# Kernel optimization log

Hardware: AMD Instinct MI355X
Metric: run time of the kernel (lower is better)

## Reference

```python
import jax, jax.numpy as jnp
import numpy as np

B, T, E = 4096, 200, 64
H = E
A = [4 * E, 80, 40]  # attn_hidden_units


def setup_inputs() -> dict:
    key = jax.random.key(0)
    ks = jax.random.split(key, 16)
    s = 0.05
    inp = {
        "gru_outputs": jax.random.normal(ks[0], (B, T, E), jnp.float32),
        "targets": jax.random.normal(ks[1], (B, 1, E), jnp.float32),
        # attention MLP: 256 -> 80 -> 40 -> 1
        "W1": jax.random.normal(ks[2], (A[0], A[1]), jnp.float32) * s,
        "b1": jnp.zeros((A[1],), jnp.float32),
        "W2": jax.random.normal(ks[3], (A[1], A[2]), jnp.float32) * s,
        "b2": jnp.zeros((A[2],), jnp.float32),
        "Wf": jax.random.normal(ks[4], (A[2], 1), jnp.float32) * s,
        "bf": jnp.zeros((1,), jnp.float32),
        # GRU cell: update/reset gates map (E+H) -> 1, candidate -> H
        "Wu": jax.random.normal(ks[5], (E + H, 1), jnp.float32) * s,
        "bu": jnp.zeros((1,), jnp.float32),
        "Wr": jax.random.normal(ks[6], (E + H, 1), jnp.float32) * s,
        "br": jnp.zeros((1,), jnp.float32),
        "Wc": jax.random.normal(ks[7], (E + H, H), jnp.float32) * s,
        "bc": jnp.zeros((H,), jnp.float32),
    }
    return inp


def reference(gru_outputs, targets, W1, b1, W2, b2, Wf, bf, Wu, bu, Wr, br, Wc, bc):
    # --- LocalActivationUnit: scores over history ---
    k = gru_outputs                                   # [B,T,E]
    q = jnp.broadcast_to(targets, k.shape)            # repeat target along T
    x = jnp.concatenate([q, k, q - k, q * k], -1)     # [B,T,4E]
    x = x @ W1 + b1                                   # (no activation in source)
    x = x @ W2 + b2
    logits = x @ Wf + bf                              # [B,T,1]
    logits = jnp.where(logits == 0, -jnp.inf, logits)  # masked_fill(logits==0, -inf)
    scores = jax.nn.softmax(logits, axis=0)           # softmax over batch dim (dim=0, as in source)

    # --- AUGRU recurrence over time ---
    def step(h, xt):
        xi, si = xt                                   # [B,E], [B,1]
        cat = jnp.concatenate([xi, h], -1)            # [B,E+H]
        u = si * jax.nn.sigmoid(cat @ Wu + bu)        # [B,1]
        r = jax.nn.sigmoid(cat @ Wr + br)             # [B,1]
        cat2 = jnp.concatenate([xi, h * r], -1)
        tilde_h = jnp.tanh(cat2 @ Wc + bc)            # [B,H]
        h = (1 - u) * h + u * tilde_h
        return h, None

    h0 = jnp.zeros((gru_outputs.shape[0], H), gru_outputs.dtype)
    xs = (jnp.swapaxes(gru_outputs, 0, 1), jnp.swapaxes(scores, 0, 1))  # [T,B,*]
    hT, _ = jax.lax.scan(step, h0, xs)
    return hT
```

## Files before the change

kernel.cpp:

```cpp
#include <hip/hip_runtime.h>
#include <hip/hip_bf16.h>
#include <math.h>

#define BB 4096
#define TT 200
#define EE 64

#define OFF_XG 1976320
#define OFF_XC 3614720
#define WS_NEED_BYTES ((size_t)(OFF_XC + (size_t)BB * TT * 64) * 4)

__device__ __forceinline__ float lane_bcast(float v, int l) {
    return __int_as_float(__builtin_amdgcn_readlane(__float_as_int(v), l));
}

__device__ __forceinline__ float dpp_ror_add(float s, const int ctrl) {
    int t;
    switch (ctrl) {
        case 8: t = __builtin_amdgcn_update_dpp(0, __float_as_int(s), 0x128, 0xF, 0xF, true); break;
        case 4: t = __builtin_amdgcn_update_dpp(0, __float_as_int(s), 0x124, 0xF, 0xF, true); break;
        case 2: t = __builtin_amdgcn_update_dpp(0, __float_as_int(s), 0x122, 0xF, 0xF, true); break;
        default: t = __builtin_amdgcn_update_dpp(0, __float_as_int(s), 0x121, 0xF, 0xF, true); break;
    }
    return s + __int_as_float(t);
}

__device__ __forceinline__ float wave_sum64(float v) {
    v = dpp_ror_add(v, 8);
    v = dpp_ror_add(v, 4);
    v = dpp_ror_add(v, 2);
    v = dpp_ror_add(v, 1);
    v += __shfl_xor(v, 16);
    v += __shfl_xor(v, 32);
    return v;
}

__global__ __launch_bounds__(128) void weff_kernel(
    const float* __restrict__ W1, const float* __restrict__ b1,
    const float* __restrict__ W2, const float* __restrict__ b2,
    const float* __restrict__ Wf, const float* __restrict__ bf,
    float* __restrict__ ws) {
    __shared__ float t80[80];
    int tid = threadIdx.x;
    if (tid < 80) {
        float s = 0.0f;
        for (int j = 0; j < 40; j++) s = fmaf(W2[tid * 40 + j], Wf[j], s);
        t80[tid] = s;
    }
    __syncthreads();
    if (tid < 64) {
        float eq = 0.f, ek = 0.f, ed = 0.f, ep = 0.f;
        for (int m = 0; m < 80; m++) {
            float t = t80[m];
            eq = fmaf(W1[tid * 80 + m],         t, eq);
            ek = fmaf(W1[(64 + tid) * 80 + m],  t, ek);
            ed = fmaf(W1[(128 + tid) * 80 + m], t, ed);
            ep = fmaf(W1[(192 + tid) * 80 + m], t, ep);
        }
        ws[tid]       = ek - ed;
        ws[64 + tid]  = ep;
        ws[128 + tid] = eq + ed;
    } else if (tid == 64) {
        float s = bf[0];
        for (int m = 0; m < 80; m++) s = fmaf(b1[m], t80[m], s);
        for (int j = 0; j < 40; j++) s = fmaf(b2[j], Wf[j], s);
        ws[192] = s;
    }
}

__global__ __launch_bounds__(256) void logits_kernel(
    const float* __restrict__ gru, const float* __restrict__ targets,
    const float* __restrict__ ws, float* __restrict__ logits) {
    __shared__ float4 sA[16], sP[16], sQ[16];
    __shared__ float sc0;
    int tid = threadIdx.x;
    if (tid < 16) {
        sA[tid] = ((const float4*)ws)[tid];
        sP[tid] = ((const float4*)(ws + 64))[tid];
        sQ[tid] = ((const float4*)(ws + 128))[tid];
    }
    if (tid == 16) sc0 = ws[192];
    __syncthreads();

    int idx = blockIdx.x * 256 + tid;
    int b = idx / 200;
    int t = idx - b * 200;
    const float4* kp = (const float4*)(gru + ((size_t)b * 200 + t) * 64);
    const float4* qp = (const float4*)(targets + (size_t)b * 64);

    float a0 = sc0, a1 = 0.f, a2 = 0.f, a3 = 0.f;
#pragma unroll
    for (int i = 0; i < 16; i++) {
        float4 kv = kp[i], qv = qp[i], A = sA[i], P = sP[i], Q = sQ[i];
        a0 = fmaf(qv.x, Q.x, a0); a0 = fmaf(kv.x, fmaf(qv.x, P.x, A.x), a0);
        a1 = fmaf(qv.y, Q.y, a1); a1 = fmaf(kv.y, fmaf(qv.y, P.y, A.y), a1);
        a2 = fmaf(qv.z, Q.z, a2); a2 = fmaf(kv.z, fmaf(qv.z, P.z, A.z), a2);
        a3 = fmaf(qv.w, Q.w, a3); a3 = fmaf(kv.w, fmaf(qv.w, P.w, A.w), a3);
    }
    float lg = (a0 + a1) + (a2 + a3);
    if (lg == 0.0f) lg = -INFINITY;
    logits[(size_t)t * BB + b] = lg;
}

__global__ __launch_bounds__(256) void softmax_kernel(const float* __restrict__ logits,
                                                      float* __restrict__ scores) {
    int t = blockIdx.x;
    int tid = threadIdx.x;
    const float* L = logits + (size_t)t * BB;
    float v[16];
#pragma unroll
    for (int i = 0; i < 16; i++) {
        float x = L[tid + i * 256];
        v[i] = (x == 0.0f) ? -INFINITY : x;
    }
    float m = v[0];
#pragma unroll
    for (int i = 1; i < 16; i++) m = fmaxf(m, v[i]);
#pragma unroll
    for (int off = 32; off; off >>= 1) m = fmaxf(m, __shfl_xor(m, off));
    __shared__ float sm[4];
    __shared__ float ss[4];
    int wid = tid >> 6;
    if ((tid & 63) == 0) sm[wid] = m;
    __syncthreads();
    m = fmaxf(fmaxf(sm[0], sm[1]), fmaxf(sm[2], sm[3]));
    float e[16];
    float s = 0.0f;
#pragma unroll
    for (int i = 0; i < 16; i++) {
        e[i] = __expf(v[i] - m);
        s += e[i];
    }
#pragma unroll
    for (int off = 32; off; off >>= 1) s += __shfl_xor(s, off);
    if ((tid & 63) == 0) ss[wid] = s;
    __syncthreads();
    s = ss[0] + ss[1] + ss[2] + ss[3];
    float inv = 1.0f / s;
    float* S = scores + (size_t)t * BB;
#pragma unroll
    for (int i = 0; i < 16; i++) S[tid + i * 256] = e[i] * inv;
}

__global__ __launch_bounds__(256) void xprep_kernel(
    const float* __restrict__ gru, const float* __restrict__ Wc,
    const float* __restrict__ bc, const float* __restrict__ Wu,
    const float* __restrict__ Wr, float* __restrict__ xc,
    float* __restrict__ xg) {
    __shared__ float  Xs[32][65];
    __shared__ float4 Ws[1024];
    __shared__ float  Wg[128];
    const int tid = threadIdx.x;
    const int n0 = blockIdx.x * 32;
    const int nl = tid >> 3;
    const int qs = tid & 7;

    const float4* Wq = (const float4*)Wc;
#pragma unroll
    for (int i = 0; i < 4; i++) Ws[tid * 4 + i] = Wq[tid * 4 + i];
    if (tid < 128) Wg[tid] = (tid < 64) ? Wu[tid] : Wr[tid - 64];
    {
        const float4* gq = (const float4*)(gru + (size_t)(n0 + nl) * 64);
        float4 aa = gq[qs * 2];
        float4 bb = gq[qs * 2 + 1];
        float* xrow = &Xs[nl][qs * 8];
        xrow[0] = aa.x; xrow[1] = aa.y; xrow[2] = aa.z; xrow[3] = aa.w;
        xrow[4] = bb.x; xrow[5] = bb.y; xrow[6] = bb.z; xrow[7] = bb.w;
    }
    __syncthreads();

    const float4* bcq = (const float4*)bc;
    float4 acc0 = bcq[qs];
    float4 acc1 = bcq[qs + 8];
#pragma unroll
    for (int k = 0; k < 64; k++) {
        float  xk = Xs[nl][k];
        float4 w0 = Ws[k * 16 + qs];
        float4 w1 = Ws[k * 16 + qs + 8];
        acc0.x = fmaf(xk, w0.x, acc0.x);
        acc0.y = fmaf(xk, w0.y, acc0.y);
        acc0.z = fmaf(xk, w0.z, acc0.z);
        acc0.w = fmaf(xk, w0.w, acc0.w);
        acc1.x = fmaf(xk, w1.x, acc1.x);
        acc1.y = fmaf(xk, w1.y, acc1.y);
        acc1.z = fmaf(xk, w1.z, acc1.z);
        acc1.w = fmaf(xk, w1.w, acc1.w);
    }
    int n = n0 + nl;
    int b = n / 200;
    int t = n - b * 200;
    float4* o = (float4*)(xc + ((size_t)t * BB + b) * 64);
    o[qs]     = acc0;
    o[qs + 8] = acc1;
    if (qs == 0) {
        float su = 0.f, sr = 0.f;
#pragma unroll
        for (int k = 0; k < 64; k++) {
            float xk = Xs[nl][k];
            su = fmaf(xk, Wg[k], su);
            sr = fmaf(xk, Wg[64 + k], sr);
        }
        ((float2*)xg)[(size_t)t * BB + b] = make_float2(su, sr);
    }
}

__global__ __launch_bounds__(256, 2) void augru2_kernel(
    const float* __restrict__ xc, const float* __restrict__ xg,
    const float* __restrict__ scores,
    const float* __restrict__ Wu, const float* __restrict__ bu,
    const float* __restrict__ Wr, const float* __restrict__ br,
    const float* __restrict__ Wc, float* __restrict__ out) {
    __shared__ float hbuf[4][64];
    const int lane = threadIdx.x & 63;
    const int wid  = threadIdx.x >> 6;
    const int b    = blockIdx.x * 4 + wid;

    float wc2[64];
#pragma unroll
    for (int k = 0; k < 64; k++) wc2[k] = Wc[(64 + k) * 64 + lane];
    const float wu2l = Wu[64 + lane];
    const float wr2l = Wr[64 + lane];
    const float sbu = bu[0], sbr = br[0];
    const float2* xg2 = (const float2*)xg;

    float h = 0.0f;
    float  x0 = xc[(size_t)b * 64 + lane];
    float2 g0 = xg2[b];
    float  s0 = scores[b];
    size_t i1 = (size_t)BB + b;
    float  x1 = xc[i1 * 64 + lane];
    float2 g1 = xg2[i1];
    float  s1 = scores[i1];

    for (int t = 0; t < TT; t++) {
        float x2 = 0.0f, s2 = 0.0f;
        float2 g2 = make_float2(0.0f, 0.0f);
        if (t + 2 < TT) {
            size_t i2 = (size_t)(t + 2) * BB + b;
            x2 = xc[i2 * 64 + lane];
            g2 = xg2[i2];
            s2 = scores[i2];
        }

        hbuf[wid][lane] = h;

        float pu = wave_sum64(h * wu2l);
        float pr = wave_sum64(h * wr2l);
        float u = s0 / (1.0f + __expf(-(pu + g0.x + sbu)));
        float r = 1.0f / (1.0f + __expf(-(pr + g0.y + sbr)));

        float a0 = 0.f, a1 = 0.f, a2 = 0.f, a3 = 0.f;
        float a4 = 0.f, a5 = 0.f, a6 = 0.f, a7 = 0.f;
        const float4* h4 = (const float4*)hbuf[wid];
#pragma unroll
        for (int kq = 0; kq < 8; kq++) {
            float4 hv0 = h4[2 * kq];
            float4 hv1 = h4[2 * kq + 1];
            a0 = fmaf(hv0.x, wc2[8 * kq + 0], a0);
            a1 = fmaf(hv0.y, wc2[8 * kq + 1], a1);
            a2 = fmaf(hv0.z, wc2[8 * kq + 2], a2);
            a3 = fmaf(hv0.w, wc2[8 * kq + 3], a3);
            a4 = fmaf(hv1.x, wc2[8 * kq + 4], a4);
            a5 = fmaf(hv1.y, wc2[8 * kq + 5], a5);
            a6 = fmaf(hv1.z, wc2[8 * kq + 6], a6);
            a7 = fmaf(hv1.w, wc2[8 * kq + 7], a7);
        }
        float cand = ((a0 + a1) + (a2 + a3)) + ((a4 + a5) + (a6 + a7));
        float arg = x0 + r * cand;
        float ex = __expf(2.0f * arg);
        float th = 1.0f - 2.0f / (ex + 1.0f);
        h = fmaf(u, th - h, h);

        x0 = x1; g0 = g1; s0 = s1;
        x1 = x2; g1 = g2; s1 = s2;
    }
    out[(size_t)b * 64 + lane] = h;
}

__global__ __launch_bounds__(128, 4) void augru_kernel(
    const float* __restrict__ gru, const float* __restrict__ scores,
    const float* __restrict__ Wu, const float* __restrict__ bu,
    const float* __restrict__ Wr, const float* __restrict__ br,
    const float* __restrict__ Wc, const float* __restrict__ bc,
    float* __restrict__ out) {
    __shared__ float sxc[2][64];
    __shared__ float sxg[2][2];
    const int lane = threadIdx.x & 63;
    const int wid  = threadIdx.x >> 6;
    const int b    = blockIdx.x;
    const float* xrow = gru + (size_t)b * TT * 64;

    if (wid == 0) {
        float wc1[64];
#pragma unroll
        for (int k = 0; k < 64; k++) wc1[k] = Wc[k * 64 + lane];
        float wu1l = Wu[lane], wr1l = Wr[lane];
        float bcl = bc[lane];

        auto produce = [&](int tp, float xl) {
            float pu = xl * wu1l;
            float pr = xl * wr1l;
#pragma unroll
            for (int off = 32; off; off >>= 1) {
                pu += __shfl_xor(pu, off);
                pr += __shfl_xor(pr, off);
            }
            float a0 = bcl, a1 = 0.0f, a2 = 0.0f, a3 = 0.0f;
#pragma unroll
            for (int k = 0; k < 16; k++) {
                a0 = fmaf(lane_bcast(xl, 4 * k + 0), wc1[4 * k + 0], a0);
                a1 = fmaf(lane_bcast(xl, 4 * k + 1), wc1[4 * k + 1], a1);
                a2 = fmaf(lane_bcast(xl, 4 * k + 2), wc1[4 * k + 2], a2);
                a3 = fmaf(lane_bcast(xl, 4 * k + 3), wc1[4 * k + 3], a3);
            }
            int p = tp & 1;
            sxc[p][lane] = (a0 + a1) + (a2 + a3);
            if (lane == 0) sxg[p][0] = pu;
            if (lane == 1) sxg[p][1] = pr;
        };

        float xl = xrow[lane];
        float xn = xrow[64 + lane];
        produce(0, xl);
        xl = xn;
        __syncthreads();
        for (int t = 0; t < TT; t++) {
            if (t + 1 < TT) {
                float xnn = (t + 2 < TT) ? xrow[(size_t)(t + 2) * 64 + lane] : 0.0f;
                produce(t + 1, xl);
                xl = xnn;
            }
            __syncthreads();
        }
    } else {
        float wc2[64];
#pragma unroll
        for (int k = 0; k < 64; k++) wc2[k] = Wc[(64 + k) * 64 + lane];
        float wu2l = Wu[64 + lane], wr2l = Wr[64 + lane];
        float sbu = bu[0], sbr = br[0];
        float h = 0.0f;
        __syncthreads();
        for (int t = 0; t < TT; t++) {
            int p = t & 1;
            float sc = scores[(size_t)t * BB + b];
            float xcv = sxc[p][lane];
            float xu = sxg[p][0];
            float xv = sxg[p][1];
            float pu = h * wu2l;
            float pr = h * wr2l;
#pragma unroll
            for (int off = 32; off; off >>= 1) {
                pu += __shfl_xor(pu, off);
                pr += __shfl_xor(pr, off);
            }
            float u = sc / (1.0f + __expf(-(pu + xu + sbu)));
            float r = 1.0f / (1.0f + __expf(-(pr + xv + sbr)));
            float a0 = 0.0f, a1 = 0.0f, a2 = 0.0f, a3 = 0.0f;
#pragma unroll
            for (int k = 0; k < 16; k++) {
                a0 = fmaf(lane_bcast(h, 4 * k + 0), wc2[4 * k + 0], a0);
                a1 = fmaf(lane_bcast(h, 4 * k + 1), wc2[4 * k + 1], a1);
                a2 = fmaf(lane_bcast(h, 4 * k + 2), wc2[4 * k + 2], a2);
                a3 = fmaf(lane_bcast(h, 4 * k + 3), wc2[4 * k + 3], a3);
            }
            float arg = xcv + r * ((a0 + a1) + (a2 + a3));
            float ex = __expf(2.0f * arg);
            float th = 1.0f - 2.0f / (ex + 1.0f);
            h = fmaf(u, th - h, h);
            __syncthreads();
        }
        out[(size_t)b * 64 + lane] = h;
    }
}

extern "C" void kernel_launch(void* const* d_in, const int* in_sizes, int n_in,
                              void* d_out, int out_size, void* d_ws, size_t ws_size,
                              hipStream_t stream) {
    const float* gru     = (const float*)d_in[0];
    const float* targets = (const float*)d_in[1];
    const float* W1 = (const float*)d_in[2];
    const float* b1 = (const float*)d_in[3];
    const float* W2 = (const float*)d_in[4];
    const float* b2 = (const float*)d_in[5];
    const float* Wf = (const float*)d_in[6];
    const float* bf = (const float*)d_in[7];
    const float* Wu = (const float*)d_in[8];
    const float* bu = (const float*)d_in[9];
    const float* Wr = (const float*)d_in[10];
    const float* br = (const float*)d_in[11];
    const float* Wc = (const float*)d_in[12];
    const float* bc = (const float*)d_in[13];
    float* out = (float*)d_out;

    float* ws     = (float*)d_ws;
    float* logits = ws + 337920;
    float* scores = ws + 1157120;

    const bool big = (ws_size >= WS_NEED_BYTES);
    float* xg = ws + OFF_XG;
    float* xc = ws + OFF_XC;

    weff_kernel<<<1, 128, 0, stream>>>(W1, b1, W2, b2, Wf, bf, ws);
    logits_kernel<<<3200, 256, 0, stream>>>(gru, targets, ws, logits);
    softmax_kernel<<<200, 256, 0, stream>>>(logits, scores);
    if (big) {
        xprep_kernel<<<25600, 256, 0, stream>>>(gru, Wc, bc, Wu, Wr, xc, xg);
        augru2_kernel<<<1024, 256, 0, stream>>>(xc, xg, scores, Wu, bu, Wr, br, Wc, out);
    } else {
        augru_kernel<<<4096, 128, 0, stream>>>(gru, scores, Wu, bu, Wr, br, Wc, bc, out);
    }
}
```

Before: 844.3 us.

## Retile input projection, store xc batch-major, stage per-row gates/scores in LDS

The input projection kernel now processes 128 rows per block, with each thread computing a 4x8 register tile using packed two-wide FMAs. It writes xc in [B][T][64] order, so the recurrence kernel streams contiguous rows per batch element instead of striding across time. The recurrence kernel preloads scores and gate projections for all 200 steps into LDS. It packs the Wc recurrent weights into v2f registers and uses packed FMAs, dropping to launch_bounds(256,1). Fewer waves per SIMD reduces latency hiding in the serial recurrence, which is the main risk.

```diff
diff --git a/kernel.cpp b/kernel.cpp
--- a/kernel.cpp
+++ b/kernel.cpp
@@ -5,6 +5,8 @@
 #define BB 4096
 #define TT 200
 #define EE 64
+
+typedef float v2f __attribute__((ext_vector_type(2)));
 
 #define OFF_XG 1976320
 #define OFF_XC 3614720
@@ -142,138 +144,178 @@
     for (int i = 0; i < 16; i++) S[tid + i * 256] = e[i] * inv;
 }
 
+#define XPAD 68
 __global__ __launch_bounds__(256) void xprep_kernel(
     const float* __restrict__ gru, const float* __restrict__ Wc,
     const float* __restrict__ bc, const float* __restrict__ Wu,
     const float* __restrict__ Wr, float* __restrict__ xc,
     float* __restrict__ xg) {
-    __shared__ float  Xs[32][65];
-    __shared__ float4 Ws[1024];
-    __shared__ float  Wg[128];
+    __shared__ float Xs[128][XPAD];
+    __shared__ float Ws[64 * 64];
     const int tid = threadIdx.x;
-    const int n0 = blockIdx.x * 32;
-    const int nl = tid >> 3;
+    const int n0 = blockIdx.x * 128;
+
+    {
+        const float4* Wq = (const float4*)Wc;
+        float4* Wsq = (float4*)Ws;
+#pragma unroll
+        for (int i = 0; i < 4; i++) Wsq[tid + 256 * i] = Wq[tid + 256 * i];
+    }
+    {
+        int row = tid >> 1, half = tid & 1;
+        const float4* gq = (const float4*)(gru + (size_t)(n0 + row) * 64 + half * 32);
+#pragma unroll
+        for (int i = 0; i < 8; i++) {
+            *(float4*)&Xs[row][half * 32 + i * 4] = gq[i];
+        }
+    }
+    __syncthreads();
+
     const int qs = tid & 7;
-
-    const float4* Wq = (const float4*)Wc;
-#pragma unroll
-    for (int i = 0; i < 4; i++) Ws[tid * 4 + i] = Wq[tid * 4 + i];
-    if (tid < 128) Wg[tid] = (tid < 64) ? Wu[tid] : Wr[tid - 64];
+    const int g  = tid >> 3;
+
+    v2f acc[4][4];
     {
-        const float4* gq = (const float4*)(gru + (size_t)(n0 + nl) * 64);
-        float4 aa = gq[qs * 2];
-        float4 bb = gq[qs * 2 + 1];
-        float* xrow = &Xs[nl][qs * 8];
-        xrow[0] = aa.x; xrow[1] = aa.y; xrow[2] = aa.z; xrow[3] = aa.w;
-        xrow[4] = bb.x; xrow[5] = bb.y; xrow[6] = bb.z; xrow[7] = bb.w;
-    }
-    __syncthreads();
-
-    const float4* bcq = (const float4*)bc;
-    float4 acc0 = bcq[qs];
-    float4 acc1 = bcq[qs + 8];
-#pragma unroll
-    for (int k = 0; k < 64; k++) {
-        float  xk = Xs[nl][k];
-        float4 w0 = Ws[k * 16 + qs];
-        float4 w1 = Ws[k * 16 + qs + 8];
-        acc0.x = fmaf(xk, w0.x, acc0.x);
-        acc0.y = fmaf(xk, w0.y, acc0.y);
-        acc0.z = fmaf(xk, w0.z, acc0.z);
-        acc0.w = fmaf(xk, w0.w, acc0.w);
-        acc1.x = fmaf(xk, w1.x, acc1.x);
-        acc1.y = fmaf(xk, w1.y, acc1.y);
-        acc1.z = fmaf(xk, w1.z, acc1.z);
-        acc1.w = fmaf(xk, w1.w, acc1.w);
-    }
-    int n = n0 + nl;
-    int b = n / 200;
-    int t = n - b * 200;
-    float4* o = (float4*)(xc + ((size_t)t * BB + b) * 64);
-    o[qs]     = acc0;
-    o[qs + 8] = acc1;
-    if (qs == 0) {
-        float su = 0.f, sr = 0.f;
-#pragma unroll
-        for (int k = 0; k < 64; k++) {
-            float xk = Xs[nl][k];
-            su = fmaf(xk, Wg[k], su);
-            sr = fmaf(xk, Wg[64 + k], sr);
-        }
-        ((float2*)xg)[(size_t)t * BB + b] = make_float2(su, sr);
-    }
-}
-
-__global__ __launch_bounds__(256, 2) void augru2_kernel(
+        const v2f* bc2 = (const v2f*)(bc + qs * 8);
+        v2f b0 = bc2[0], b1 = bc2[1], b2v = bc2[2], b3 = bc2[3];
+#pragma unroll
+        for (int ri = 0; ri < 4; ri++) {
+            acc[ri][0] = b0; acc[ri][1] = b1; acc[ri][2] = b2v; acc[ri][3] = b3;
+        }
+    }
+
+#pragma unroll 4
+    for (int kc = 0; kc < 16; kc++) {
+        float4 xr[4];
+#pragma unroll
+        for (int ri = 0; ri < 4; ri++)
+            xr[ri] = *(const float4*)&Xs[g + 32 * ri][kc * 4];
+#pragma unroll
+        for (int kk = 0; kk < 4; kk++) {
+            const float4* wq = (const float4*)&Ws[(kc * 4 + kk) * 64 + qs * 8];
+            float4 wa = wq[0], wb = wq[1];
+            v2f w0 = {wa.x, wa.y}, w1 = {wa.z, wa.w};
+            v2f w2 = {wb.x, wb.y}, w3 = {wb.z, wb.w};
+#pragma unroll
+            for (int ri = 0; ri < 4; ri++) {
+                float xv = (kk == 0) ? xr[ri].x : (kk == 1) ? xr[ri].y
+                         : (kk == 2) ? xr[ri].z : xr[ri].w;
+                v2f xb = {xv, xv};
+                acc[ri][0] = __builtin_elementwise_fma(xb, w0, acc[ri][0]);
+                acc[ri][1] = __builtin_elementwise_fma(xb, w1, acc[ri][1]);
+                acc[ri][2] = __builtin_elementwise_fma(xb, w2, acc[ri][2]);
+                acc[ri][3] = __builtin_elementwise_fma(xb, w3, acc[ri][3]);
+            }
+        }
+    }
+
+#pragma unroll
+    for (int ri = 0; ri < 4; ri++) {
+        int n = n0 + g + 32 * ri;
+        float4 o0 = {acc[ri][0].x, acc[ri][0].y, acc[ri][1].x, acc[ri][1].y};
+        float4 o1 = {acc[ri][2].x, acc[ri][2].y, acc[ri][3].x, acc[ri][3].y};
+        float4* o = (float4*)(xc + (size_t)n * 64 + qs * 8);
+        o[0] = o0;
+        o[1] = o1;
+    }
+
+    {
+        int m = qs & 3;
+        int row = g + 32 * m;
+        const float* wsel = (qs >> 2) ? Wr : Wu;
+        const float4* wq = (const float4*)wsel;
+        float d0 = 0.f, d1 = 0.f, d2 = 0.f, d3 = 0.f;
+#pragma unroll
+        for (int i = 0; i < 16; i++) {
+            float4 xv = *(const float4*)&Xs[row][i * 4];
+            float4 wv = wq[i];
+            d0 = fmaf(xv.x, wv.x, d0);
+            d1 = fmaf(xv.y, wv.y, d1);
+            d2 = fmaf(xv.z, wv.z, d2);
+            d3 = fmaf(xv.w, wv.w, d3);
+        }
+        float dot = (d0 + d1) + (d2 + d3);
+        int n = n0 + row;
+        xg[(size_t)n * 2 + (qs >> 2)] = dot;
+    }
+}
+
+__global__ __launch_bounds__(256, 1) void augru3_kernel(
     const float* __restrict__ xc, const float* __restrict__ xg,
     const float* __restrict__ scores,
     const float* __restrict__ Wu, const float* __restrict__ bu,
     const float* __restrict__ Wr, const float* __restrict__ br,
     const float* __restrict__ Wc, float* __restrict__ out) {
-    __shared__ float hbuf[4][64];
+    __shared__ float  hbuf[4][64];
+    __shared__ float  ssc[4][200];
+    __shared__ float2 sxgl[4][200];
     const int lane = threadIdx.x & 63;
     const int wid  = threadIdx.x >> 6;
     const int b    = blockIdx.x * 4 + wid;
 
-    float wc2[64];
-#pragma unroll
-    for (int k = 0; k < 64; k++) wc2[k] = Wc[(64 + k) * 64 + lane];
+    const float2* xg2 = (const float2*)xg;
+    for (int t0 = lane; t0 < TT; t0 += 64) {
+        ssc[wid][t0]  = scores[(size_t)t0 * BB + b];
+        sxgl[wid][t0] = xg2[(size_t)b * TT + t0];
+    }
+
+    v2f wc[32];
+#pragma unroll
+    for (int m = 0; m < 32; m++) {
+        wc[m].x = Wc[(64 + 2 * m) * 64 + lane];
+        wc[m].y = Wc[(64 + 2 * m + 1) * 64 + lane];
+    }
     const float wu2l = Wu[64 + lane];
     const float wr2l = Wr[64 + lane];
     const float sbu = bu[0], sbr = br[0];
-    const float2* xg2 = (const float2*)xg;
 
     float h = 0.0f;
-    float  x0 = xc[(size_t)b * 64 + lane];
-    float2 g0 = xg2[b];
-    float  s0 = scores[b];
-    size_t i1 = (size_t)BB + b;
-    float  x1 = xc[i1 * 64 + lane];
-    float2 g1 = xg2[i1];
-    float  s1 = scores[i1];
-
-    for (int t = 0; t < TT; t++) {
-        float x2 = 0.0f, s2 = 0.0f;
-        float2 g2 = make_float2(0.0f, 0.0f);
-        if (t + 2 < TT) {
-            size_t i2 = (size_t)(t + 2) * BB + b;
-            x2 = xc[i2 * 64 + lane];
-            g2 = xg2[i2];
-            s2 = scores[i2];
-        }
-
-        hbuf[wid][lane] = h;
-
+    float* hb = hbuf[wid];
+    const float4* h4 = (const float4*)hb;
+    const float* ssw = ssc[wid];
+    const float2* sxw = sxgl[wid];
+
+    auto step = [&](int t, float xl) {
+        hb[lane] = h;
         float pu = wave_sum64(h * wu2l);
         float pr = wave_sum64(h * wr2l);
-        float u = s0 / (1.0f + __expf(-(pu + g0.x + sbu)));
-        float r = 1.0f / (1.0f + __expf(-(pr + g0.y + sbr)));
-
-        float a0 = 0.f, a1 = 0.f, a2 = 0.f, a3 = 0.f;
-        float a4 = 0.f, a5 = 0.f, a6 = 0.f, a7 = 0.f;
-        const float4* h4 = (const float4*)hbuf[wid];
-#pragma unroll
-        for (int kq = 0; kq < 8; kq++) {
-            float4 hv0 = h4[2 * kq];
-            float4 hv1 = h4[2 * kq + 1];
-            a0 = fmaf(hv0.x, wc2[8 * kq + 0], a0);
-            a1 = fmaf(hv0.y, wc2[8 * kq + 1], a1);
-            a2 = fmaf(hv0.z, wc2[8 * kq + 2], a2);
-            a3 = fmaf(hv0.w, wc2[8 * kq + 3], a3);
-            a4 = fmaf(hv1.x, wc2[8 * kq + 4], a4);
-            a5 = fmaf(hv1.y, wc2[8 * kq + 5], a5);
-            a6 = fmaf(hv1.z, wc2[8 * kq + 6], a6);
-            a7 = fmaf(hv1.w, wc2[8 * kq + 7], a7);
-        }
-        float cand = ((a0 + a1) + (a2 + a3)) + ((a4 + a5) + (a6 + a7));
-        float arg = x0 + r * cand;
+        float sc = ssw[t];
+        float2 gg = sxw[t];
+        float u = sc / (1.0f + __expf(-(pu + gg.x + sbu)));
+        float r = 1.0f / (1.0f + __expf(-(pr + gg.y + sbr)));
+
+        v2f a0 = {0.f, 0.f}, a1 = a0, a2 = a0, a3 = a0;
+#pragma unroll
+        for (int q = 0; q < 16; q += 2) {
+            float4 hA = h4[q], hB = h4[q + 1];
+            v2f hA0 = {hA.x, hA.y}, hA1 = {hA.z, hA.w};
+            v2f hB0 = {hB.x, hB.y}, hB1 = {hB.z, hB.w};
+            a0 = __builtin_elementwise_fma(hA0, wc[2 * q],     a0);
+            a1 = __builtin_elementwise_fma(hA1, wc[2 * q + 1], a1);
+            a2 = __builtin_elementwise_fma(hB0, wc[2 * q + 2], a2);
+            a3 = __builtin_elementwise_fma(hB1, wc[2 * q + 3], a3);
+        }
+        v2f sv = (a0 + a1) + (a2 + a3);
+        float cand = sv.x + sv.y;
+
+        float arg = xl + r * cand;
         float ex = __expf(2.0f * arg);
         float th = 1.0f - 2.0f / (ex + 1.0f);
         h = fmaf(u, th - h, h);
-
-        x0 = x1; g0 = g1; s0 = s1;
-        x1 = x2; g1 = g2; s1 = s2;
-    }
+    };
+
+    const float* xp = xc + (size_t)b * TT * 64 + lane;
+    float x0 = xp[0];
+    float x1 = xp[64];
+    for (int t = 0; t < TT - 2; t++) {
+        float x2 = xp[128];
+        xp += 64;
+        step(t, x0);
+        x0 = x1; x1 = x2;
+    }
+    step(TT - 2, x0);
+    step(TT - 1, x1);
+
     out[(size_t)b * 64 + lane] = h;
 }
 
@@ -404,8 +446,8 @@
     logits_kernel<<<3200, 256, 0, stream>>>(gru, targets, ws, logits);
     softmax_kernel<<<200, 256, 0, stream>>>(logits, scores);
     if (big) {
-        xprep_kernel<<<25600, 256, 0, stream>>>(gru, Wc, bc, Wu, Wr, xc, xg);
-        augru2_kernel<<<1024, 256, 0, stream>>>(xc, xg, scores, Wu, bu, Wr, br, Wc, out);
+        xprep_kernel<<<6400, 256, 0, stream>>>(gru, Wc, bc, Wu, Wr, xc, xg);
+        augru3_kernel<<<1024, 256, 0, stream>>>(xc, xg, scores, Wu, bu, Wr, br, Wc, out);
     } else {
         augru_kernel<<<4096, 128, 0, stream>>>(gru, scores, Wu, bu, Wr, br, Wc, bc, out);
     }
```

Result: faster. 691.0 us (-18.2%).
